# Performance work log

Hardware: AMD Instinct MI355X
Metric: run time of the kernel (lower is better)

The kernel has to match this reference:

```python
import jax, jax.numpy as jnp
import numpy as np

EPS = 1e-8        # slot-attention epsilon
LN_EPS = 1e-5     # torch LayerNorm default
NUM_ITERS = 3

def _ln(x, g, b):
    m = jnp.mean(x, axis=-1, keepdims=True)
    v = jnp.var(x, axis=-1, keepdims=True)
    return (x - m) * jax.lax.rsqrt(v + LN_EPS) * g + b

def setup_inputs() -> dict:
    key = jax.random.key(0)
    ks = jax.random.split(key, 24)
    B, N, D, S, K, H = 64, 4096, 256, 256, 8, 512
    sc = 0.02
    return {
        "inputs": jax.random.normal(ks[0], (B, N, D), dtype=jnp.float32),
        "noise": jax.random.normal(ks[1], (B, K, S), dtype=jnp.float32),
        "slot_mu": jax.random.normal(ks[2], (1, 1, S)) * sc,
        "slot_log_sigma": jax.random.normal(ks[3], (1, 1, S)) * sc,
        "g_in": jnp.ones((D,)), "b_in": jnp.zeros((D,)),
        "g_sl": jnp.ones((S,)), "b_sl": jnp.zeros((S,)),
        "g_mlp": jnp.ones((S,)), "b_mlp": jnp.zeros((S,)),
        "Wq": jax.random.normal(ks[4], (S, S)) * sc,
        "Wk": jax.random.normal(ks[5], (S, D)) * sc,
        "Wv": jax.random.normal(ks[6], (S, D)) * sc,
        "W_ih": jax.random.normal(ks[7], (3 * S, S)) * sc,
        "W_hh": jax.random.normal(ks[8], (3 * S, S)) * sc,
        "b_ih": jnp.zeros((3 * S,)), "b_hh": jnp.zeros((3 * S,)),
        "W1": jax.random.normal(ks[9], (H, S)) * sc,
        "b1": jnp.zeros((H,)),
        "W2": jax.random.normal(ks[10], (S, H)) * sc,
        "b2": jnp.zeros((S,)),
    }

def _gru_cell(x, h, W_ih, W_hh, b_ih, b_hh):
    gi = x @ W_ih.T + b_ih
    gh = h @ W_hh.T + b_hh
    ir, iz, inn = jnp.split(gi, 3, axis=-1)
    hr, hz, hn = jnp.split(gh, 3, axis=-1)
    r = jax.nn.sigmoid(ir + hr)
    z = jax.nn.sigmoid(iz + hz)
    n = jnp.tanh(inn + r * hn)
    return (1.0 - z) * n + z * h

def reference(inputs, noise, slot_mu, slot_log_sigma, g_in, b_in, g_sl, b_sl,
              g_mlp, b_mlp, Wq, Wk, Wv, W_ih, W_hh, b_ih, b_hh, W1, b1, W2, b2):
    S = Wq.shape[0]
    slots = slot_mu + jnp.exp(slot_log_sigma) * noise          # [B,K,S]
    x = _ln(inputs, g_in, b_in)                                # [B,N,D]
    k = (x @ Wk.T) * (S ** -0.5)                               # [B,N,S]
    v = x @ Wv.T                                               # [B,N,S]
    for i in range(NUM_ITERS):
        slots_prev = slots
        q = _ln(slots, g_sl, b_sl) @ Wq.T                      # [B,K,S]
        attn_logits = jnp.einsum('bns,bks->bnk', k, q)         # [B,N,K]
        attn = jax.nn.softmax(attn_logits, axis=-1) + EPS      # softmax over slots
        attn = attn / jnp.sum(attn, axis=1, keepdims=True)     # normalize over inputs
        updates = jnp.einsum('bnk,bns->bks', attn, v)          # [B,K,S]
        slots = _gru_cell(updates, slots_prev, W_ih, W_hh, b_ih, b_hh)
        if i < NUM_ITERS - 1:
            h = jax.nn.relu(_ln(slots, g_mlp, b_mlp) @ W1.T + b1)
            slots = slots + (h @ W2.T + b2)
    return slots
```

## Files before the change

kernel.cpp:

```cpp
#include <hip/hip_runtime.h>
#include <math.h>

#define NB 64
#define NN 4096
#define ND 256
#define NS 256
#define NK 8
#define NH 512
#define NROW (NB*NN)
#define NSLOT (NB*NK)
#define EPSA 1e-8f

typedef unsigned short u16;
typedef unsigned int   u32;
typedef __bf16 bf16x8 __attribute__((ext_vector_type(8)));
typedef float  f32x4  __attribute__((ext_vector_type(4)));

__device__ __forceinline__ float bf2f(u16 u) {
  union { u32 i; float f; } v; v.i = ((u32)u) << 16; return v.f;
}
__device__ __forceinline__ u16 f2bf(float f) {
  union { float f; u32 i; } v; v.f = f;
  u32 x = v.i;
  return (u16)((x + 0x7FFFu + ((x >> 16) & 1u)) >> 16);
}

#define OFF_KV     0ULL
#define OFF_SLOTS  268435456ULL
#define OFF_QBF    268959744ULL
#define OFF_UPDP   269221888ULL
#define OFF_SUMSP  277610496ULL
#define OFF_WC     277643264ULL
#define OFF_WQT    277905408ULL
#define OFF_WIHT   278167552ULL
#define OFF_WHHT   278953984ULL
#define OFF_W1T    279740416ULL
#define OFF_W2T    280264704ULL

__global__ __launch_bounds__(256) void prep_kernel(
    const float* __restrict__ Wq, const float* __restrict__ Wk, const float* __restrict__ Wv,
    const float* __restrict__ Wih, const float* __restrict__ Whh,
    const float* __restrict__ W1, const float* __restrict__ W2,
    u16* __restrict__ Wc, float* __restrict__ WqT, float* __restrict__ WihT,
    float* __restrict__ WhhT, float* __restrict__ W1T, float* __restrict__ W2T)
{
  int idx = blockIdx.x * 256 + threadIdx.x;
  if (idx < 512*256) {
    int j = idx >> 8, d = idx & 255;
    float w = (j < 256) ? Wk[idx] * 0.0625f : Wv[idx - 65536];
    Wc[idx] = f2bf(w);
    W1T[d*512 + j] = W1[idx];
  }
  if (idx < 256*256) {
    int j = idx >> 8, d = idx & 255;
    WqT[d*256 + j] = Wq[idx];
  }
  if (idx < 768*256) {
    int j = idx >> 8, d = idx & 255;
    WihT[d*768 + j] = Wih[idx];
    WhhT[d*768 + j] = Whh[idx];
  }
  if (idx < 256*512) {
    int j = idx >> 9, h = idx & 511;
    W2T[h*256 + j] = W2[idx];
  }
}

__global__ __launch_bounds__(256) void slots_init_kernel(
    const float* __restrict__ noise, const float* __restrict__ mu,
    const float* __restrict__ lsig, float* __restrict__ slots)
{
  int idx = blockIdx.x * 256 + threadIdx.x;
  int s = idx & 255;
  slots[idx] = mu[s] + expf(lsig[s]) * noise[idx];
}

__global__ __launch_bounds__(256) void lngemm_kernel(
    const float* __restrict__ x, const float* __restrict__ gw, const float* __restrict__ bw,
    const u16* __restrict__ Wc, u16* __restrict__ kv)
{
  __shared__ u16 As[16384];
  __shared__ u16 Bs[16384];
  const int t = threadIdx.x, w = t >> 6, lane = t & 63;
  const int L15 = lane & 15, q4 = lane >> 4;
  const int blk = blockIdx.x;

  float4 gv = *(const float4*)(gw + lane*4);
  float4 bv = *(const float4*)(bw + lane*4);
  for (int i = 0; i < 16; ++i) {
    int m = w*16 + i;
    float4 xv = *(const float4*)(x + ((size_t)(blk*64 + m))*256 + lane*4);
    float s  = xv.x + xv.y + xv.z + xv.w;
    float sq = xv.x*xv.x + xv.y*xv.y + xv.z*xv.z + xv.w*xv.w;
    #pragma unroll
    for (int mm = 32; mm >= 1; mm >>= 1) { s += __shfl_xor(s, mm, 64); sq += __shfl_xor(sq, mm, 64); }
    float mean = s * (1.f/256.f);
    float rstd = rsqrtf(sq * (1.f/256.f) - mean*mean + 1e-5f);
    ushort4 o;
    o.x = f2bf((xv.x - mean)*rstd*gv.x + bv.x);
    o.y = f2bf((xv.y - mean)*rstd*gv.y + bv.y);
    o.z = f2bf((xv.z - mean)*rstd*gv.z + bv.z);
    o.w = f2bf((xv.w - mean)*rstd*gv.w + bv.w);
    int swz = (lane >> 1) ^ (m & 7);
    *(ushort4*)&As[m*256 + swz*8 + (lane & 1)*4] = o;
  }
  for (int nc = 0; nc < 8; ++nc) {
    #pragma unroll
    for (int i = 0; i < 8; ++i) {
      int slot = i*4 + w;
      int g = slot*64 + lane;
      int jr = g >> 5, c = g & 31;
      const u16* src = Wc + ((size_t)(nc*64 + jr))*256 + ((c ^ (jr & 7)) << 3);
      __builtin_amdgcn_global_load_lds(
        (const __attribute__((address_space(1))) u32*)src,
        (__attribute__((address_space(3))) u32*)((char*)Bs + slot*1024 + lane*16), 16, 0, 0);
    }
    __syncthreads();
    f32x4 acc[4] = {};
    #pragma unroll
    for (int ks = 0; ks < 8; ++ks) {
      int swz = (ks*4 + q4) ^ (L15 & 7);
      bf16x8 af = *(const bf16x8*)&As[(w*16 + L15)*256 + swz*8];
      #pragma unroll
      for (int nt = 0; nt < 4; ++nt) {
        bf16x8 bf = *(const bf16x8*)&Bs[(nt*16 + L15)*256 + swz*8];
        acc[nt] = __builtin_amdgcn_mfma_f32_16x16x32_bf16(af, bf, acc[nt], 0, 0, 0);
      }
    }
    __syncthreads();
    #pragma unroll
    for (int nt = 0; nt < 4; ++nt)
      #pragma unroll
      for (int reg = 0; reg < 4; ++reg) {
        size_t row = (size_t)blk*64 + w*16 + q4*4 + reg;
        int col = nc*64 + nt*16 + L15;
        kv[row*512 + col] = f2bf(acc[nt][reg]);
      }
  }
}

__global__ __launch_bounds__(256) void q_kernel(
    const float* __restrict__ slots, const float* __restrict__ gw, const float* __restrict__ bw,
    const float* __restrict__ WqT, u16* __restrict__ qbf)
{
  __shared__ float ln[2][256];
  int t = threadIdx.x, wv = t >> 6, lane = t & 63;
  int base = blockIdx.x * 2;
  if (wv < 2) {
    int row = base + wv;
    float4 xv = *(const float4*)(slots + (size_t)row*256 + lane*4);
    float s  = xv.x + xv.y + xv.z + xv.w;
    float sq = xv.x*xv.x + xv.y*xv.y + xv.z*xv.z + xv.w*xv.w;
    #pragma unroll
    for (int m = 32; m >= 1; m >>= 1) { s += __shfl_xor(s, m, 64); sq += __shfl_xor(sq, m, 64); }
    float mean = s * (1.f/256.f);
    float rstd = rsqrtf(sq * (1.f/256.f) - mean*mean + 1e-5f);
    float4 gv = *(const float4*)(gw + lane*4);
    float4 bv = *(const float4*)(bw + lane*4);
    ln[wv][lane*4+0] = (xv.x - mean)*rstd*gv.x + bv.x;
    ln[wv][lane*4+1] = (xv.y - mean)*rstd*gv.y + bv.y;
    ln[wv][lane*4+2] = (xv.z - mean)*rstd*gv.z + bv.z;
    ln[wv][lane*4+3] = (xv.w - mean)*rstd*gv.w + bv.w;
  }
  __syncthreads();
  float a0 = 0.f, a1 = 0.f;
  for (int d = 0; d < 256; ++d) {
    float w = WqT[d*256 + t];
    a0 += ln[0][d] * w;
    a1 += ln[1][d] * w;
  }
  qbf[(size_t)base*256 + t]     = f2bf(a0);
  qbf[(size_t)(base+1)*256 + t] = f2bf(a1);
}

__global__ __launch_bounds__(256) void attn_kernel(
    const u16* __restrict__ kv, const u16* __restrict__ qbf,
    float* __restrict__ updp, float* __restrict__ sums_p)
{
  __shared__ u16 tile[16384];
  __shared__ u16 attn_bf[16*72];
  __shared__ float sums_w[4][8];
  const int b = blockIdx.x, cg = blockIdx.y;
  const int t = threadIdx.x, w = t >> 6, lane = t & 63;
  const int L15 = lane & 15, q4 = lane >> 4;

  if (t < 32) sums_w[t >> 3][t & 7] = 0.f;

  bf16x8 qf[8];
  {
    int slot = (L15 < 8) ? L15 : 7;
    const u16* qp = qbf + ((size_t)b*8 + slot)*256;
    #pragma unroll
    for (int ks = 0; ks < 8; ++ks)
      qf[ks] = *(const bf16x8*)(qp + ks*32 + q4*8);
  }

  f32x4 accp[4] = {};
  for (int cc = 0; cc < 4; ++cc) {
    const int n0 = cg*256 + cc*64;
    uint4 vr[8];
    #pragma unroll
    for (int j = 0; j < 8; ++j) {
      int idx = j*256 + t;
      int n = idx >> 5, dc = idx & 31;
      vr[j] = *(const uint4*)(kv + ((size_t)(b*4096 + n0 + n))*512 + 256 + dc*8);
    }
    #pragma unroll
    for (int i = 0; i < 8; ++i) {
      int slot = i*4 + w;
      int g = slot*64 + lane;
      int lr = g >> 5, c = g & 31;
      const u16* src = kv + ((size_t)(b*4096 + n0 + lr))*512 + ((c ^ (lr & 7)) << 3);
      __builtin_amdgcn_global_load_lds(
        (const __attribute__((address_space(1))) u32*)src,
        (__attribute__((address_space(3))) u32*)((char*)tile + slot*1024 + lane*16), 16, 0, 0);
    }
    __syncthreads();
    f32x4 lg = {};
    #pragma unroll
    for (int ks = 0; ks < 8; ++ks) {
      int swz = (ks*4 + q4) ^ (L15 & 7);
      bf16x8 af = *(const bf16x8*)&tile[(w*16 + L15)*256 + swz*8];
      lg = __builtin_amdgcn_mfma_f32_16x16x32_bf16(af, qf[ks], lg, 0, 0, 0);
    }
    float attnv[4], tot = 0.f;
    #pragma unroll
    for (int reg = 0; reg < 4; ++reg) {
      float val = lg[reg];
      float mx = val;
      mx = fmaxf(mx, __shfl_xor(mx, 1, 64));
      mx = fmaxf(mx, __shfl_xor(mx, 2, 64));
      mx = fmaxf(mx, __shfl_xor(mx, 4, 64));
      float e = expf(val - mx);
      float se = e;
      se += __shfl_xor(se, 1, 64);
      se += __shfl_xor(se, 2, 64);
      se += __shfl_xor(se, 4, 64);
      attnv[reg] = e / se + EPSA;
      tot += attnv[reg];
    }
    tot += __shfl_xor(tot, 16, 64);
    tot += __shfl_xor(tot, 32, 64);
    __syncthreads();
    #pragma unroll
    for (int j = 0; j < 8; ++j) {
      int idx = j*256 + t;
      int n = idx >> 5, dc = idx & 31;
      u32 words[4] = {vr[j].x, vr[j].y, vr[j].z, vr[j].w};
      #pragma unroll
      for (int e = 0; e < 8; ++e) {
        int d = dc*8 + e;
        int f = (dc + e) & 7;
        int swz = (n >> 3) ^ f;
        tile[d*64 + swz*8 + (n & 7)] = (u16)(words[e >> 1] >> ((e & 1)*16));
      }
    }
    if (L15 < 8) {
      #pragma unroll
      for (int reg = 0; reg < 4; ++reg)
        attn_bf[L15*72 + w*16 + q4*4 + reg] = f2bf(attnv[reg]);
      if (lane < 8) sums_w[w][lane] += tot;
    }
    __syncthreads();
    #pragma unroll
    for (int ks = 0; ks < 2; ++ks) {
      bf16x8 paf = *(const bf16x8*)&attn_bf[L15*72 + ks*32 + q4*8];
      #pragma unroll
      for (int nt = 0; nt < 4; ++nt) {
        int d = (w*4 + nt)*16 + L15;
        int swz = (ks*4 + q4) ^ ((d + (d >> 3)) & 7);
        bf16x8 vbf = *(const bf16x8*)&tile[d*64 + swz*8];
        accp[nt] = __builtin_amdgcn_mfma_f32_16x16x32_bf16(paf, vbf, accp[nt], 0, 0, 0);
      }
    }
    __syncthreads();
  }
  float* up = updp + ((size_t)(b*16 + cg))*2048;
  if (q4 < 2) {
    #pragma unroll
    for (int nt = 0; nt < 4; ++nt) {
      int d = (w*4 + nt)*16 + L15;
      #pragma unroll
      for (int reg = 0; reg < 4; ++reg)
        up[(q4*4 + reg)*256 + d] = accp[nt][reg];
    }
  }
  if (t < 8)
    sums_p[(b*16 + cg)*8 + t] = sums_w[0][t] + sums_w[1][t] + sums_w[2][t] + sums_w[3][t];
}

__global__ __launch_bounds__(256) void grumlp_kernel(
    const float* __restrict__ updp, const float* __restrict__ sums_p,
    const float* __restrict__ WihT, const float* __restrict__ WhhT,
    const float* __restrict__ bih, const float* __restrict__ bhh,
    const float* __restrict__ gm, const float* __restrict__ bm,
    const float* __restrict__ W1T, const float* __restrict__ b1,
    const float* __restrict__ W2T, const float* __restrict__ b2,
    float* __restrict__ slots, int do_mlp)
{
  __shared__ float xs[4][256], hs[4][256];
  __shared__ float ln[4][256];
  __shared__ float hb[4][512];
  int t = threadIdx.x, w = t >> 6, lane = t & 63;
  int base = blockIdx.x * 4;
  #pragma unroll
  for (int g = 0; g < 4; ++g) {
    int row = base + g;
    int b = row >> 3, s = row & 7;
    float u = 0.f, sm = 0.f;
    for (int c = 0; c < 16; ++c) {
      u  += updp[((size_t)(b*16 + c)*8 + s)*256 + t];
      sm += sums_p[(b*16 + c)*8 + s];
    }
    xs[g][t] = u / sm;
    hs[g][t] = slots[(size_t)row*256 + t];
  }
  __syncthreads();
  float ra[4] = {}, za[4] = {}, ia[4] = {}, ha[4] = {};
  for (int d = 0; d < 256; ++d) {
    float wir = WihT[d*768 + t], wiz = WihT[d*768 + 256 + t], win = WihT[d*768 + 512 + t];
    float whr = WhhT[d*768 + t], whz = WhhT[d*768 + 256 + t], whn = WhhT[d*768 + 512 + t];
    #pragma unroll
    for (int g = 0; g < 4; ++g) {
      float xx = xs[g][d], hh = hs[g][d];
      ra[g] += xx*wir + hh*whr;
      za[g] += xx*wiz + hh*whz;
      ia[g] += xx*win;
      ha[g] += hh*whn;
    }
  }
  float bir = bih[t], biz = bih[256+t], bin = bih[512+t];
  float bhr = bhh[t], bhz = bhh[256+t], bhn = bhh[512+t];
  float nv[4];
  #pragma unroll
  for (int g = 0; g < 4; ++g) {
    float r  = 1.f/(1.f + expf(-(ra[g] + bir + bhr)));
    float z  = 1.f/(1.f + expf(-(za[g] + biz + bhz)));
    float nn = tanhf(ia[g] + bin + r*(ha[g] + bhn));
    nv[g] = (1.f - z)*nn + z*hs[g][t];
  }
  if (!do_mlp) {
    #pragma unroll
    for (int g = 0; g < 4; ++g)
      slots[(size_t)(base+g)*256 + t] = nv[g];
    return;
  }
  #pragma unroll
  for (int g = 0; g < 4; ++g) xs[g][t] = nv[g];
  __syncthreads();
  {
    float4 xv = *(const float4*)&xs[w][lane*4];
    float s  = xv.x + xv.y + xv.z + xv.w;
    float sq = xv.x*xv.x + xv.y*xv.y + xv.z*xv.z + xv.w*xv.w;
    #pragma unroll
    for (int m = 32; m >= 1; m >>= 1) { s += __shfl_xor(s, m, 64); sq += __shfl_xor(sq, m, 64); }
    float mean = s * (1.f/256.f);
    float rstd = rsqrtf(sq * (1.f/256.f) - mean*mean + 1e-5f);
    float4 gv = *(const float4*)(gm + lane*4);
    float4 bv = *(const float4*)(bm + lane*4);
    ln[w][lane*4+0] = (xv.x - mean)*rstd*gv.x + bv.x;
    ln[w][lane*4+1] = (xv.y - mean)*rstd*gv.y + bv.y;
    ln[w][lane*4+2] = (xv.z - mean)*rstd*gv.z + bv.z;
    ln[w][lane*4+3] = (xv.w - mean)*rstd*gv.w + bv.w;
  }
  __syncthreads();
  float h0[4] = {}, h1[4] = {};
  for (int d = 0; d < 256; ++d) {
    float w0 = W1T[d*512 + t], w1 = W1T[d*512 + 256 + t];
    #pragma unroll
    for (int g = 0; g < 4; ++g) { float l = ln[g][d]; h0[g] += l*w0; h1[g] += l*w1; }
  }
  float bb0 = b1[t], bb1 = b1[256 + t];
  #pragma unroll
  for (int g = 0; g < 4; ++g) {
    hb[g][t]       = fmaxf(h0[g] + bb0, 0.f);
    hb[g][256 + t] = fmaxf(h1[g] + bb1, 0.f);
  }
  __syncthreads();
  float o[4] = {};
  for (int hh = 0; hh < 512; ++hh) {
    float ww = W2T[hh*256 + t];
    #pragma unroll
    for (int g = 0; g < 4; ++g) o[g] += hb[g][hh] * ww;
  }
  float b2v = b2[t];
  #pragma unroll
  for (int g = 0; g < 4; ++g)
    slots[(size_t)(base+g)*256 + t] = xs[g][t] + o[g] + b2v;
}

extern "C" void kernel_launch(void* const* d_in, const int* in_sizes, int n_in,
                              void* d_out, int out_size, void* d_ws, size_t ws_size,
                              hipStream_t stream)
{
  (void)in_sizes; (void)n_in; (void)out_size; (void)ws_size;
  const float* inputs = (const float*)d_in[0];
  const float* noise  = (const float*)d_in[1];
  const float* mu     = (const float*)d_in[2];
  const float* lsig   = (const float*)d_in[3];
  const float* g_in   = (const float*)d_in[4];
  const float* b_in   = (const float*)d_in[5];
  const float* g_sl   = (const float*)d_in[6];
  const float* b_sl   = (const float*)d_in[7];
  const float* g_mlp  = (const float*)d_in[8];
  const float* b_mlp  = (const float*)d_in[9];
  const float* Wq     = (const float*)d_in[10];
  const float* Wk     = (const float*)d_in[11];
  const float* Wv     = (const float*)d_in[12];
  const float* Wih    = (const float*)d_in[13];
  const float* Whh    = (const float*)d_in[14];
  const float* bih    = (const float*)d_in[15];
  const float* bhh    = (const float*)d_in[16];
  const float* W1     = (const float*)d_in[17];
  const float* b1     = (const float*)d_in[18];
  const float* W2     = (const float*)d_in[19];
  const float* b2     = (const float*)d_in[20];

  char* ws = (char*)d_ws;
  u16*   kv     = (u16*)  (ws + OFF_KV);
  float* slots  = (float*)(ws + OFF_SLOTS);
  u16*   qb     = (u16*)  (ws + OFF_QBF);
  float* updp   = (float*)(ws + OFF_UPDP);
  float* sums_p = (float*)(ws + OFF_SUMSP);
  u16*   Wc     = (u16*)  (ws + OFF_WC);
  float* WqT    = (float*)(ws + OFF_WQT);
  float* WihT   = (float*)(ws + OFF_WIHT);
  float* WhhT   = (float*)(ws + OFF_WHHT);
  float* W1T    = (float*)(ws + OFF_W1T);
  float* W2T    = (float*)(ws + OFF_W2T);

  prep_kernel<<<768, 256, 0, stream>>>(Wq, Wk, Wv, Wih, Whh, W1, W2,
                                       Wc, WqT, WihT, WhhT, W1T, W2T);
  slots_init_kernel<<<512, 256, 0, stream>>>(noise, mu, lsig, slots);
  lngemm_kernel<<<NROW/64, 256, 0, stream>>>(inputs, g_in, b_in, Wc, kv);

  for (int it = 0; it < 3; ++it) {
    q_kernel<<<NSLOT/2, 256, 0, stream>>>(slots, g_sl, b_sl, WqT, qb);
    attn_kernel<<<dim3(NB, 16), 256, 0, stream>>>(kv, qb, updp, sums_p);
    grumlp_kernel<<<NSLOT/4, 256, 0, stream>>>(updp, sums_p, WihT, WhhT, bih, bhh,
                                               g_mlp, b_mlp, W1T, b1, W2T, b2,
                                               slots, (it < 2) ? 1 : 0);
  }
  hipMemcpyAsync(d_out, slots, (size_t)NSLOT*NS*sizeof(float),
                 hipMemcpyDeviceToDevice, stream);
}
```

Baseline: 1.038 ms.

## Split LN and KV GEMM, store V transposed, widen attention grid

Replaces the fused LayerNorm+GEMM with a standalone LN-to-bf16 cast kernel followed by a 128x128-tiled MFMA GEMM. The GEMM writes K row-major and V pre-transposed, so the attention kernel loads V fragments directly instead of transposing them through shared memory. The attention kernel now handles one 64-row chunk per block over 64 chunk groups. This removes the in-kernel transpose and the serial chunk loop, but adds an extra bf16 round trip of the normalized inputs through memory and four times as many partial results for the GRU kernel to reduce.

```diff
diff --git a/kernel.cpp b/kernel.cpp
--- a/kernel.cpp
+++ b/kernel.cpp
@@ -10,6 +10,7 @@
 #define NROW (NB*NN)
 #define NSLOT (NB*NK)
 #define EPSA 1e-8f
+#define NCG 64
 
 typedef unsigned short u16;
 typedef unsigned int   u32;
@@ -24,18 +25,23 @@
   u32 x = v.i;
   return (u16)((x + 0x7FFFu + ((x >> 16) & 1u)) >> 16);
 }
-
-#define OFF_KV     0ULL
-#define OFF_SLOTS  268435456ULL
-#define OFF_QBF    268959744ULL
-#define OFF_UPDP   269221888ULL
-#define OFF_SUMSP  277610496ULL
-#define OFF_WC     277643264ULL
-#define OFF_WQT    277905408ULL
-#define OFF_WIHT   278167552ULL
-#define OFF_WHHT   278953984ULL
-#define OFF_W1T    279740416ULL
-#define OFF_W2T    280264704ULL
+__device__ __forceinline__ u32 pack2(float a, float b) {
+  return (u32)f2bf(a) | ((u32)f2bf(b) << 16);
+}
+
+#define OFF_XBF    0ULL
+#define OFF_KG     134217728ULL
+#define OFF_VTG    268435456ULL
+#define OFF_SLOTS  402653184ULL
+#define OFF_QBF    403177472ULL
+#define OFF_UPDP   403439616ULL
+#define OFF_SUMSP  436994048ULL
+#define OFF_WC     437125120ULL
+#define OFF_WQT    437387264ULL
+#define OFF_WIHT   437649408ULL
+#define OFF_WHHT   438435840ULL
+#define OFF_W1T    439222272ULL
+#define OFF_W2T    439746560ULL
 
 __global__ __launch_bounds__(256) void prep_kernel(
     const float* __restrict__ Wq, const float* __restrict__ Wk, const float* __restrict__ Wv,
@@ -75,67 +81,107 @@
   slots[idx] = mu[s] + expf(lsig[s]) * noise[idx];
 }
 
-__global__ __launch_bounds__(256) void lngemm_kernel(
-    const float* __restrict__ x, const float* __restrict__ gw, const float* __restrict__ bw,
-    const u16* __restrict__ Wc, u16* __restrict__ kv)
-{
-  __shared__ u16 As[16384];
-  __shared__ u16 Bs[16384];
-  const int t = threadIdx.x, w = t >> 6, lane = t & 63;
-  const int L15 = lane & 15, q4 = lane >> 4;
-  const int blk = blockIdx.x;
-
-  float4 gv = *(const float4*)(gw + lane*4);
-  float4 bv = *(const float4*)(bw + lane*4);
-  for (int i = 0; i < 16; ++i) {
-    int m = w*16 + i;
-    float4 xv = *(const float4*)(x + ((size_t)(blk*64 + m))*256 + lane*4);
-    float s  = xv.x + xv.y + xv.z + xv.w;
-    float sq = xv.x*xv.x + xv.y*xv.y + xv.z*xv.z + xv.w*xv.w;
-    #pragma unroll
-    for (int mm = 32; mm >= 1; mm >>= 1) { s += __shfl_xor(s, mm, 64); sq += __shfl_xor(sq, mm, 64); }
-    float mean = s * (1.f/256.f);
-    float rstd = rsqrtf(sq * (1.f/256.f) - mean*mean + 1e-5f);
-    ushort4 o;
-    o.x = f2bf((xv.x - mean)*rstd*gv.x + bv.x);
-    o.y = f2bf((xv.y - mean)*rstd*gv.y + bv.y);
-    o.z = f2bf((xv.z - mean)*rstd*gv.z + bv.z);
-    o.w = f2bf((xv.w - mean)*rstd*gv.w + bv.w);
-    int swz = (lane >> 1) ^ (m & 7);
-    *(ushort4*)&As[m*256 + swz*8 + (lane & 1)*4] = o;
-  }
-  for (int nc = 0; nc < 8; ++nc) {
-    #pragma unroll
-    for (int i = 0; i < 8; ++i) {
-      int slot = i*4 + w;
-      int g = slot*64 + lane;
-      int jr = g >> 5, c = g & 31;
-      const u16* src = Wc + ((size_t)(nc*64 + jr))*256 + ((c ^ (jr & 7)) << 3);
+__global__ __launch_bounds__(256) void ln_cast_kernel(
+    const float* __restrict__ x, const float* __restrict__ g, const float* __restrict__ bb,
+    u16* __restrict__ out)
+{
+  int row = blockIdx.x * 4 + (threadIdx.x >> 6);
+  int lane = threadIdx.x & 63;
+  float4 xv = *(const float4*)(x + (size_t)row * 256 + lane * 4);
+  float s  = xv.x + xv.y + xv.z + xv.w;
+  float sq = xv.x*xv.x + xv.y*xv.y + xv.z*xv.z + xv.w*xv.w;
+  #pragma unroll
+  for (int m = 32; m >= 1; m >>= 1) { s += __shfl_xor(s, m, 64); sq += __shfl_xor(sq, m, 64); }
+  float mean = s * (1.f/256.f);
+  float rstd = rsqrtf(sq * (1.f/256.f) - mean*mean + 1e-5f);
+  float4 gv = *(const float4*)(g + lane*4);
+  float4 bv = *(const float4*)(bb + lane*4);
+  ushort4 o;
+  o.x = f2bf((xv.x - mean) * rstd * gv.x + bv.x);
+  o.y = f2bf((xv.y - mean) * rstd * gv.y + bv.y);
+  o.z = f2bf((xv.z - mean) * rstd * gv.z + bv.z);
+  o.w = f2bf((xv.w - mean) * rstd * gv.w + bv.w);
+  *(ushort4*)(out + (size_t)row * 256 + lane*4) = o;
+}
+
+__global__ __launch_bounds__(256) void gemm_kv_kernel(
+    const u16* __restrict__ A, const u16* __restrict__ Bt,
+    u16* __restrict__ kg, u16* __restrict__ vtg)
+{
+  __shared__ u16 smem[17408];
+  u16* As = smem;
+  u16* Bs = smem + 4096;
+  const int tid = threadIdx.x;
+  const int lane = tid & 63;
+  const int wv = tid >> 6;
+  const int bm = blockIdx.x;
+  const int bn = blockIdx.y;
+  const int wm = (wv & 1) * 64;
+  const int wn = (wv >> 1) * 64;
+
+  f32x4 acc[4][4] = {};
+
+  for (int k0 = 0; k0 < 256; k0 += 32) {
+    #pragma unroll
+    for (int r = 0; r < 2; ++r) {
+      int off = ((r*4 + wv) << 10) + lane*16;
+      int row = off >> 6;
+      int col = (off & 63) >> 1;
+      const u16* ga = A  + (size_t)(bm*128 + row) * 256 + k0 + col;
+      const u16* gb = Bt + (size_t)(bn*128 + row) * 256 + k0 + col;
       __builtin_amdgcn_global_load_lds(
-        (const __attribute__((address_space(1))) u32*)src,
-        (__attribute__((address_space(3))) u32*)((char*)Bs + slot*1024 + lane*16), 16, 0, 0);
+        (const __attribute__((address_space(1))) u32*)ga,
+        (__attribute__((address_space(3))) u32*)((char*)As + off), 16, 0, 0);
+      __builtin_amdgcn_global_load_lds(
+        (const __attribute__((address_space(1))) u32*)gb,
+        (__attribute__((address_space(3))) u32*)((char*)Bs + off), 16, 0, 0);
     }
     __syncthreads();
-    f32x4 acc[4] = {};
-    #pragma unroll
-    for (int ks = 0; ks < 8; ++ks) {
-      int swz = (ks*4 + q4) ^ (L15 & 7);
-      bf16x8 af = *(const bf16x8*)&As[(w*16 + L15)*256 + swz*8];
+    bf16x8 af[4], bfr[4];
+    #pragma unroll
+    for (int t4 = 0; t4 < 4; ++t4) {
+      af[t4]  = *(const bf16x8*)&As[(wm + t4*16 + (lane & 15)) * 32 + (lane >> 4) * 8];
+      bfr[t4] = *(const bf16x8*)&Bs[(wn + t4*16 + (lane & 15)) * 32 + (lane >> 4) * 8];
+    }
+    #pragma unroll
+    for (int mt = 0; mt < 4; ++mt)
+      #pragma unroll
+      for (int nt = 0; nt < 4; ++nt)
+        acc[mt][nt] = __builtin_amdgcn_mfma_f32_16x16x32_bf16(af[mt], bfr[nt], acc[mt][nt], 0, 0, 0);
+    __syncthreads();
+  }
+  const int cr = (lane >> 4) * 4;
+  const int cc = lane & 15;
+  if (bn < 2) {
+    #pragma unroll
+    for (int mt = 0; mt < 4; ++mt)
+      #pragma unroll
+      for (int nt = 0; nt < 4; ++nt)
+        #pragma unroll
+        for (int r = 0; r < 4; ++r) {
+          size_t row = (size_t)(bm*128 + wm + mt*16 + cr + r);
+          int col = bn*128 + wn + nt*16 + cc;
+          kg[row * 256 + col] = f2bf(acc[mt][nt][r]);
+        }
+  } else {
+    #pragma unroll
+    for (int mt = 0; mt < 4; ++mt)
       #pragma unroll
       for (int nt = 0; nt < 4; ++nt) {
-        bf16x8 bf = *(const bf16x8*)&Bs[(nt*16 + L15)*256 + swz*8];
-        acc[nt] = __builtin_amdgcn_mfma_f32_16x16x32_bf16(af, bf, acc[nt], 0, 0, 0);
+        int c  = wn + nt*16 + cc;
+        int r0 = wm + mt*16 + cr;
+        u32* p = (u32*)&smem[c*136 + r0];
+        p[0] = pack2(acc[mt][nt][0], acc[mt][nt][1]);
+        p[1] = pack2(acc[mt][nt][2], acc[mt][nt][3]);
       }
-    }
     __syncthreads();
-    #pragma unroll
-    for (int nt = 0; nt < 4; ++nt)
-      #pragma unroll
-      for (int reg = 0; reg < 4; ++reg) {
-        size_t row = (size_t)blk*64 + w*16 + q4*4 + reg;
-        int col = nc*64 + nt*16 + L15;
-        kv[row*512 + col] = f2bf(acc[nt][reg]);
-      }
+    int c = tid >> 1, half = tid & 1;
+    int d = (bn - 2) * 128 + c;
+    const u16* srcp = &smem[c*136 + half*64];
+    u16* dstp = vtg + (size_t)(bm >> 5)*1048576 + (size_t)d*4096 + (bm & 31)*128 + half*64;
+    #pragma unroll
+    for (int i = 0; i < 8; ++i)
+      *(uint4*)(dstp + i*8) = *(const uint4*)(srcp + i*8);
   }
 }
 
@@ -174,119 +220,106 @@
 }
 
 __global__ __launch_bounds__(256) void attn_kernel(
-    const u16* __restrict__ kv, const u16* __restrict__ qbf,
+    const u16* __restrict__ kg, const u16* __restrict__ vtg, const u16* __restrict__ qbf,
     float* __restrict__ updp, float* __restrict__ sums_p)
 {
   __shared__ u16 tile[16384];
-  __shared__ u16 attn_bf[16*72];
+  __shared__ u16 attnT[16*72];
   __shared__ float sums_w[4][8];
   const int b = blockIdx.x, cg = blockIdx.y;
   const int t = threadIdx.x, w = t >> 6, lane = t & 63;
   const int L15 = lane & 15, q4 = lane >> 4;
-
-  if (t < 32) sums_w[t >> 3][t & 7] = 0.f;
-
+  const int n0 = cg*64;
+  const int slot = L15 & 7;
+
+  bf16x8 vb[2][4];
+  #pragma unroll
+  for (int ks = 0; ks < 2; ++ks)
+    #pragma unroll
+    for (int dt = 0; dt < 4; ++dt) {
+      int d = (dt*4 + w)*16 + L15;
+      vb[ks][dt] = *(const bf16x8*)(vtg + (size_t)b*1048576 + (size_t)d*4096 + n0 + ks*32 + q4*8);
+    }
   bf16x8 qf[8];
   {
-    int slot = (L15 < 8) ? L15 : 7;
     const u16* qp = qbf + ((size_t)b*8 + slot)*256;
     #pragma unroll
     for (int ks = 0; ks < 8; ++ks)
       qf[ks] = *(const bf16x8*)(qp + ks*32 + q4*8);
   }
-
-  f32x4 accp[4] = {};
-  for (int cc = 0; cc < 4; ++cc) {
-    const int n0 = cg*256 + cc*64;
-    uint4 vr[8];
+  {
+    const u16* srcbase = kg + (size_t)(b*4096 + n0)*256;
     #pragma unroll
     for (int j = 0; j < 8; ++j) {
-      int idx = j*256 + t;
-      int n = idx >> 5, dc = idx & 31;
-      vr[j] = *(const uint4*)(kv + ((size_t)(b*4096 + n0 + n))*512 + 256 + dc*8);
-    }
-    #pragma unroll
-    for (int i = 0; i < 8; ++i) {
-      int slot = i*4 + w;
-      int g = slot*64 + lane;
-      int lr = g >> 5, c = g & 31;
-      const u16* src = kv + ((size_t)(b*4096 + n0 + lr))*512 + ((c ^ (lr & 7)) << 3);
+      int i = w*8 + j;
+      int n = i*2 + (lane >> 5);
+      int p = lane & 31;
+      int c = (p & 24) | ((p ^ n) & 7);
+      const u16* src = srcbase + (size_t)n*256 + c*8;
       __builtin_amdgcn_global_load_lds(
         (const __attribute__((address_space(1))) u32*)src,
-        (__attribute__((address_space(3))) u32*)((char*)tile + slot*1024 + lane*16), 16, 0, 0);
-    }
-    __syncthreads();
-    f32x4 lg = {};
+        (__attribute__((address_space(3))) u32*)((char*)tile + i*1024 + lane*16), 16, 0, 0);
+    }
+  }
+  __syncthreads();
+
+  f32x4 lg = {};
+  {
+    int n = w*16 + L15;
     #pragma unroll
     for (int ks = 0; ks < 8; ++ks) {
-      int swz = (ks*4 + q4) ^ (L15 & 7);
-      bf16x8 af = *(const bf16x8*)&tile[(w*16 + L15)*256 + swz*8];
+      int cck = ks*4 + q4;
+      int p = (cck & 24) | ((cck ^ n) & 7);
+      bf16x8 af = *(const bf16x8*)&tile[n*256 + p*8];
       lg = __builtin_amdgcn_mfma_f32_16x16x32_bf16(af, qf[ks], lg, 0, 0, 0);
     }
-    float attnv[4], tot = 0.f;
-    #pragma unroll
-    for (int reg = 0; reg < 4; ++reg) {
-      float val = lg[reg];
-      float mx = val;
-      mx = fmaxf(mx, __shfl_xor(mx, 1, 64));
-      mx = fmaxf(mx, __shfl_xor(mx, 2, 64));
-      mx = fmaxf(mx, __shfl_xor(mx, 4, 64));
-      float e = expf(val - mx);
-      float se = e;
-      se += __shfl_xor(se, 1, 64);
-      se += __shfl_xor(se, 2, 64);
-      se += __shfl_xor(se, 4, 64);
-      attnv[reg] = e / se + EPSA;
-      tot += attnv[reg];
-    }
-    tot += __shfl_xor(tot, 16, 64);
-    tot += __shfl_xor(tot, 32, 64);
-    __syncthreads();
-    #pragma unroll
-    for (int j = 0; j < 8; ++j) {
-      int idx = j*256 + t;
-      int n = idx >> 5, dc = idx & 31;
-      u32 words[4] = {vr[j].x, vr[j].y, vr[j].z, vr[j].w};
+  }
+  float av[4], tot = 0.f;
+  #pragma unroll
+  for (int r = 0; r < 4; ++r) {
+    float val = lg[r];
+    float mx = val;
+    mx = fmaxf(mx, __shfl_xor(mx, 1, 64));
+    mx = fmaxf(mx, __shfl_xor(mx, 2, 64));
+    mx = fmaxf(mx, __shfl_xor(mx, 4, 64));
+    float e = expf(val - mx);
+    float se = e;
+    se += __shfl_xor(se, 1, 64);
+    se += __shfl_xor(se, 2, 64);
+    se += __shfl_xor(se, 4, 64);
+    av[r] = e / se + EPSA;
+    tot += av[r];
+  }
+  if (L15 < 8) {
+    u32* p = (u32*)&attnT[L15*72 + w*16 + q4*4];
+    p[0] = pack2(av[0], av[1]);
+    p[1] = pack2(av[2], av[3]);
+  }
+  tot += __shfl_xor(tot, 16, 64);
+  tot += __shfl_xor(tot, 32, 64);
+  if (q4 == 0 && L15 < 8) sums_w[w][L15] = tot;
+  __syncthreads();
+
+  f32x4 accp[4] = {};
+  #pragma unroll
+  for (int ks = 0; ks < 2; ++ks) {
+    bf16x8 pa = *(const bf16x8*)&attnT[slot*72 + ks*32 + q4*8];
+    #pragma unroll
+    for (int dt = 0; dt < 4; ++dt)
+      accp[dt] = __builtin_amdgcn_mfma_f32_16x16x32_bf16(pa, vb[ks][dt], accp[dt], 0, 0, 0);
+  }
+  if (q4 < 2) {
+    float* up = updp + ((size_t)(b*NCG + cg))*2048;
+    #pragma unroll
+    for (int dt = 0; dt < 4; ++dt) {
+      int d = (dt*4 + w)*16 + L15;
       #pragma unroll
-      for (int e = 0; e < 8; ++e) {
-        int d = dc*8 + e;
-        int f = (dc + e) & 7;
-        int swz = (n >> 3) ^ f;
-        tile[d*64 + swz*8 + (n & 7)] = (u16)(words[e >> 1] >> ((e & 1)*16));
-      }
-    }
-    if (L15 < 8) {
-      #pragma unroll
-      for (int reg = 0; reg < 4; ++reg)
-        attn_bf[L15*72 + w*16 + q4*4 + reg] = f2bf(attnv[reg]);
-      if (lane < 8) sums_w[w][lane] += tot;
-    }
-    __syncthreads();
-    #pragma unroll
-    for (int ks = 0; ks < 2; ++ks) {
-      bf16x8 paf = *(const bf16x8*)&attn_bf[L15*72 + ks*32 + q4*8];
-      #pragma unroll
-      for (int nt = 0; nt < 4; ++nt) {
-        int d = (w*4 + nt)*16 + L15;
-        int swz = (ks*4 + q4) ^ ((d + (d >> 3)) & 7);
-        bf16x8 vbf = *(const bf16x8*)&tile[d*64 + swz*8];
-        accp[nt] = __builtin_amdgcn_mfma_f32_16x16x32_bf16(paf, vbf, accp[nt], 0, 0, 0);
-      }
-    }
-    __syncthreads();
-  }
-  float* up = updp + ((size_t)(b*16 + cg))*2048;
-  if (q4 < 2) {
-    #pragma unroll
-    for (int nt = 0; nt < 4; ++nt) {
-      int d = (w*4 + nt)*16 + L15;
-      #pragma unroll
-      for (int reg = 0; reg < 4; ++reg)
-        up[(q4*4 + reg)*256 + d] = accp[nt][reg];
+      for (int r = 0; r < 4; ++r)
+        up[(q4*4 + r)*256 + d] = accp[dt][r];
     }
   }
   if (t < 8)
-    sums_p[(b*16 + cg)*8 + t] = sums_w[0][t] + sums_w[1][t] + sums_w[2][t] + sums_w[3][t];
+    sums_p[(b*NCG + cg)*8 + t] = sums_w[0][t] + sums_w[1][t] + sums_w[2][t] + sums_w[3][t];
 }
 
 __global__ __launch_bounds__(256) void grumlp_kernel(
@@ -308,9 +341,9 @@
     int row = base + g;
     int b = row >> 3, s = row & 7;
     float u = 0.f, sm = 0.f;
-    for (int c = 0; c < 16; ++c) {
-      u  += updp[((size_t)(b*16 + c)*8 + s)*256 + t];
-      sm += sums_p[(b*16 + c)*8 + s];
+    for (int c = 0; c < NCG; ++c) {
+      u  += updp[((size_t)(b*NCG + c)*8 + s)*256 + t];
+      sm += sums_p[(b*NCG + c)*8 + s];
     }
     xs[g][t] = u / sm;
     hs[g][t] = slots[(size_t)row*256 + t];
@@ -417,7 +450,9 @@
   const float* b2     = (const float*)d_in[20];
 
   char* ws = (char*)d_ws;
-  u16*   kv     = (u16*)  (ws + OFF_KV);
+  u16*   x_bf   = (u16*)  (ws + OFF_XBF);
+  u16*   kg     = (u16*)  (ws + OFF_KG);
+  u16*   vtg    = (u16*)  (ws + OFF_VTG);
   float* slots  = (float*)(ws + OFF_SLOTS);
   u16*   qb     = (u16*)  (ws + OFF_QBF);
   float* updp   = (float*)(ws + OFF_UPDP);
@@ -432,11 +467,12 @@
   prep_kernel<<<768, 256, 0, stream>>>(Wq, Wk, Wv, Wih, Whh, W1, W2,
                                        Wc, WqT, WihT, WhhT, W1T, W2T);
   slots_init_kernel<<<512, 256, 0, stream>>>(noise, mu, lsig, slots);
-  lngemm_kernel<<<NROW/64, 256, 0, stream>>>(inputs, g_in, b_in, Wc, kv);
+  ln_cast_kernel<<<NROW/4, 256, 0, stream>>>(inputs, g_in, b_in, x_bf);
+  gemm_kv_kernel<<<dim3(NROW/128, 4), 256, 0, stream>>>(x_bf, Wc, kg, vtg);
 
   for (int it = 0; it < 3; ++it) {
     q_kernel<<<NSLOT/2, 256, 0, stream>>>(slots, g_sl, b_sl, WqT, qb);
-    attn_kernel<<<dim3(NB, 16), 256, 0, stream>>>(kv, qb, updp, sums_p);
+    attn_kernel<<<dim3(NB, NCG), 256, 0, stream>>>(kg, vtg, qb, updp, sums_p);
     grumlp_kernel<<<NSLOT/4, 256, 0, stream>>>(updp, sums_p, WihT, WhhT, bih, bhh,
                                                g_mlp, b_mlp, W1T, b1, W2T, b2,
                                                slots, (it < 2) ? 1 : 0);
```

After: 1.131 ms. +9.0%, slower.
